# Performance work log

Measured on AMD Instinct MI355X. Metric: run time of the kernel, lower is better.

## Reference

```python
import jax, jax.numpy as jnp
import numpy as np

B, C, H, W = 2048, 256, 7, 7
EPS = 1e-6  # torch.nn.CosineSimilarity eps


def _masked_cos_loss(f1, f2, A):
    """Fused all-pairs masked cosine similarity.
    f1, f2: [B, C, H, W]; A: [H, W, H, W] binary mask.
    Replaces the original 7x7x7x7 Python loop of per-pixel CosineSimilarity calls.
    Returns per-batch loss [B]: sum_{ijkl: A==1} cos(f1[:,:,i,j], f2[:,:,k,l]) / (H*W*H*W).
    """
    n1 = jnp.linalg.norm(f1, axis=1)  # [B, H, W]
    n2 = jnp.linalg.norm(f2, axis=1)  # [B, H, W]
    dot = jnp.einsum('bcij,bckl->bijkl', f1, f2)  # [B, H, W, H, W]
    denom = jnp.maximum(n1[:, :, :, None, None] * n2[:, None, None, :, :], EPS)
    cos = dot / denom
    mask = (A == 1).astype(f1.dtype)
    return jnp.einsum('bijkl,ijkl->b', cos, mask) / (H * W * H * W)


def setup_inputs() -> dict:
    key = jax.random.key(0)
    k1, k2, k3, k4 = jax.random.split(key, 4)
    base_feature = jax.random.normal(k1, (B, C, H, W), dtype=jnp.float32)
    moment_feature = jax.random.normal(k2, (B, C, H, W), dtype=jnp.float32)
    base_A = jax.random.randint(k3, (H, W, H, W), 0, 2, dtype=jnp.int32)
    moment_A = jax.random.randint(k4, (H, W, H, W), 0, 2, dtype=jnp.int32)
    return {"base_feature": base_feature, "moment_feature": moment_feature,
            "base_A": base_A, "moment_A": moment_A}


def reference(base_feature, moment_feature, base_A, moment_A):
    # base_loss  = masked cos(base[i,j],   moment[k,l]) under base_A
    # moment_loss = masked cos(moment[i,j], base[k,l])  under moment_A
    base_loss = _masked_cos_loss(base_feature, moment_feature, base_A)
    moment_loss = _masked_cos_loss(moment_feature, base_feature, moment_A)
    return -base_loss - moment_loss  # [B]
```

## Files before the change

kernel.cpp:

```cpp
#include <hip/hip_runtime.h>
#include <math.h>


constexpr int NB     = 2048;
constexpr int NC     = 256;
constexpr int NP     = 49;
constexpr int SLAB_C = 8;
constexpr int PITCH  = 12;
constexpr int FWORDS = NP * PITCH;
constexpr int REGION = 1280;
constexpr int NSLABW = (NC / 2) / SLAB_C;
constexpr float EPS  = 1e-6f;

__global__ __launch_bounds__(256, 2)
void pixpro_kernel(const float* __restrict__ gbase,
                   const float* __restrict__ gmom,
                   const int*   __restrict__ A1,
                   const int*   __restrict__ A2,
                   float*       __restrict__ out)
{
    __shared__ unsigned char wtb[NP * NP];
    __shared__ __align__(16) float slab[4][REGION];

    const int tid  = threadIdx.x;
    const int wave = tid >> 6;
    const int lane = tid & 63;
    const int b    = blockIdx.x * 2 + (wave >> 1);
    const int half = wave & 1;

    for (int t = tid; t < NP * NP; t += 256) {
        int p = t / NP, q = t - p * NP;
        wtb[t] = (unsigned char)((A1[t] == 1 ? 1 : 0) + (A2[q * NP + p] == 1 ? 1 : 0));
    }
    __syncthreads();

    float* const sl  = slab[wave];
    float* const slb = sl;
    float* const slm = sl + FWORDS;

    const int lp = lane & 7, lq = lane >> 3;
    const int p0 = (lp < 7 ? lp : 6) * 7;
    const int q0 = (lq < 7 ? lq : 6) * 7;

    const float* gb = gbase + (size_t)b * (NC * NP) + (size_t)half * (128 * NP);
    const float* gm = gmom  + (size_t)b * (NC * NP) + (size_t)half * (128 * NP);

    const bool ld = (lane < NP);

    int wof[4];
    #pragma unroll
    for (int u = 0; u < 4; ++u) {
        int e  = 4 * lane + u;
        wof[u] = (e - 49 * (e / 49)) * PITCH + (e / 49);
    }

    const float* const vA = (lane < NP) ? (slb + lane * PITCH)
                                        : (slm + (lane - NP) * PITCH);
    const float* const vB = slm + ((lane < 34) ? (15 + lane) : 48) * PITCH;
    const float* const bp = slb + p0 * PITCH;
    const float* const mp = slm + q0 * PITCH;

    float acc[7][7];
    #pragma unroll
    for (int j = 0; j < 7; ++j)
        #pragma unroll
        for (int i = 0; i < 7; ++i) acc[j][i] = 0.0f;
    float nrm0 = 0.0f, nrm1 = 0.0f;

    float4 rb0 = {}, rb1 = {}, rm0 = {}, rm1 = {};
    if (ld) {
        const float4* pb = (const float4*)gb;
        const float4* pm = (const float4*)gm;
        rb0 = pb[lane]; rb1 = pb[lane + NP];
        rm0 = pm[lane]; rm1 = pm[lane + NP];
    }

    for (int s = 0; s < NSLABW; ++s) {
        if (ld) {
            slb[wof[0]]     = rb0.x; slb[wof[1]]     = rb0.y; slb[wof[2]]     = rb0.z; slb[wof[3]]     = rb0.w;
            slb[wof[0] + 4] = rb1.x; slb[wof[1] + 4] = rb1.y; slb[wof[2] + 4] = rb1.z; slb[wof[3] + 4] = rb1.w;
            slm[wof[0]]     = rm0.x; slm[wof[1]]     = rm0.y; slm[wof[2]]     = rm0.z; slm[wof[3]]     = rm0.w;
            slm[wof[0] + 4] = rm1.x; slm[wof[1] + 4] = rm1.y; slm[wof[2] + 4] = rm1.z; slm[wof[3] + 4] = rm1.w;
        }
        if (s + 1 < NSLABW && ld) {
            const float4* pb = (const float4*)(gb + (s + 1) * (SLAB_C * NP));
            const float4* pm = (const float4*)(gm + (s + 1) * (SLAB_C * NP));
            rb0 = pb[lane]; rb1 = pb[lane + NP];
            rm0 = pm[lane]; rm1 = pm[lane + NP];
        }
        asm volatile("s_waitcnt lgkmcnt(0)" ::: "memory");

        #pragma unroll
        for (int c0 = 0; c0 < SLAB_C; c0 += 4) {
            float4 mv[7];
            #pragma unroll
            for (int j = 0; j < 7; ++j)
                mv[j] = *(const float4*)(mp + j * PITCH + c0);
            float4 a4 = *(const float4*)(vA + c0);
            float4 b4 = *(const float4*)(vB + c0);
            nrm0 = fmaf(a4.x, a4.x, fmaf(a4.y, a4.y, fmaf(a4.z, a4.z, fmaf(a4.w, a4.w, nrm0))));
            nrm1 = fmaf(b4.x, b4.x, fmaf(b4.y, b4.y, fmaf(b4.z, b4.z, fmaf(b4.w, b4.w, nrm1))));
            #pragma unroll
            for (int i = 0; i < 7; ++i) {
                float4 bv = *(const float4*)(bp + i * PITCH + c0);
                #pragma unroll
                for (int j = 0; j < 7; ++j) {
                    float t0 = fmaf(bv.x, mv[j].x, acc[j][i]);
                    t0       = fmaf(bv.y, mv[j].y, t0);
                    t0       = fmaf(bv.z, mv[j].z, t0);
                    acc[j][i] = fmaf(bv.w, mv[j].w, t0);
                }
            }
        }
        asm volatile("s_waitcnt lgkmcnt(0)" ::: "memory");
    }

    __syncthreads();

    float* const ex   = slab[wave & ~1];
    const bool active = (lp < 7) && (lq < 7);
    const int  tix    = lq * 7 + lp;

    if (half) {
        ex[lane]      = nrm0;
        ex[64 + lane] = nrm1;
        if (active) {
            #pragma unroll
            for (int j = 0; j < 7; ++j)
                #pragma unroll
                for (int i = 0; i < 7; ++i)
                    ex[128 + tix * 49 + j * 7 + i] = acc[j][i];
        }
    }
    __syncthreads();

    if (!half) {
        nrm0 += ex[lane];
        nrm1 += ex[64 + lane];
        if (active) {
            #pragma unroll
            for (int j = 0; j < 7; ++j)
                #pragma unroll
                for (int i = 0; i < 7; ++i)
                    acc[j][i] += ex[128 + tix * 49 + j * 7 + i];
        }
        asm volatile("s_waitcnt lgkmcnt(0)" ::: "memory");

        ex[lane] = nrm0;
        if (lane < 34) ex[64 + lane] = nrm1;
        asm volatile("s_waitcnt lgkmcnt(0)" ::: "memory");

        float nbv[7], nmv[7];
        #pragma unroll
        for (int i = 0; i < 7; ++i) nbv[i] = sqrtf(ex[p0 + i]);
        #pragma unroll
        for (int j = 0; j < 7; ++j) nmv[j] = sqrtf(ex[NP + q0 + j]);

        float sum = 0.0f;
        if (active) {
            #pragma unroll
            for (int j = 0; j < 7; ++j)
                #pragma unroll
                for (int i = 0; i < 7; ++i) {
                    float w     = (float)wtb[(p0 + i) * NP + (q0 + j)];
                    float denom = fmaxf(nbv[i] * nmv[j], EPS);
                    sum += w * acc[j][i] / denom;
                }
        }
        #pragma unroll
        for (int m = 32; m; m >>= 1) sum += __shfl_xor(sum, m, 64);
        if (lane == 0) out[b] = sum * (-1.0f / 2401.0f);
    }
}

extern "C" void kernel_launch(void* const* d_in, const int* in_sizes, int n_in,
                              void* d_out, int out_size, void* d_ws, size_t ws_size,
                              hipStream_t stream)
{
    (void)in_sizes; (void)n_in; (void)d_ws; (void)ws_size; (void)out_size;
    const float* base = (const float*)d_in[0];
    const float* mom  = (const float*)d_in[1];
    const int*   A1   = (const int*)d_in[2];
    const int*   A2   = (const int*)d_in[3];
    float*       out  = (float*)d_out;

    pixpro_kernel<<<NB / 2, 256, 0, stream>>>(base, mom, A1, A2, out);
}
```

Measured before the change: 262.5 us.

## Double-buffer 4-channel LDS slabs with per-lane strided loads, dropping transpose scatter

Shrinks the per-wave LDS slab to 4 channels and keeps two LDS buffers (A and B) with their own register prefetches two slabs ahead. Each lane now loads one pixel's 4 channels with scalar strided global loads and stores them as one float4 into a pixel-major layout with pitch 4. This replaces the eight scattered scalar LDS writes of the old transpose. The goal is to cut LDS store instructions and bank conflicts and to overlap global loads with compute. In exchange, the global loads are no longer vectorised: each lane issues 4 separate dword loads per slab instead of 2 float4 loads.

```diff
diff --git a/kernel.cpp b/kernel.cpp
--- a/kernel.cpp
+++ b/kernel.cpp
@@ -5,9 +5,9 @@
 constexpr int NB     = 2048;
 constexpr int NC     = 256;
 constexpr int NP     = 49;
-constexpr int SLAB_C = 8;
-constexpr int PITCH  = 12;
-constexpr int FWORDS = NP * PITCH;
+constexpr int SLAB_C = 4;
+constexpr int FW     = NP * SLAB_C;
+constexpr int BUFW   = 2 * FW;
 constexpr int REGION = 1280;
 constexpr int NSLABW = (NC / 2) / SLAB_C;
 constexpr float EPS  = 1e-6f;
@@ -34,9 +34,7 @@
     }
     __syncthreads();
 
-    float* const sl  = slab[wave];
-    float* const slb = sl;
-    float* const slm = sl + FWORDS;
+    float* const sl = slab[wave];
 
     const int lp = lane & 7, lq = lane >> 3;
     const int p0 = (lp < 7 ? lp : 6) * 7;
@@ -44,21 +42,13 @@
 
     const float* gb = gbase + (size_t)b * (NC * NP) + (size_t)half * (128 * NP);
     const float* gm = gmom  + (size_t)b * (NC * NP) + (size_t)half * (128 * NP);
+    const float* gbl = gb + lane;
+    const float* gml = gm + lane;
 
     const bool ld = (lane < NP);
 
-    int wof[4];
-    #pragma unroll
-    for (int u = 0; u < 4; ++u) {
-        int e  = 4 * lane + u;
-        wof[u] = (e - 49 * (e / 49)) * PITCH + (e / 49);
-    }
-
-    const float* const vA = (lane < NP) ? (slb + lane * PITCH)
-                                        : (slm + (lane - NP) * PITCH);
-    const float* const vB = slm + ((lane < 34) ? (15 + lane) : 48) * PITCH;
-    const float* const bp = slb + p0 * PITCH;
-    const float* const mp = slm + q0 * PITCH;
+    const int vAw = (lane < NP) ? (4 * lane) : (FW + 4 * (lane - NP));
+    const int vBw = FW + 4 * ((lane < 34) ? (15 + lane) : 48);
 
     float acc[7][7];
     #pragma unroll
@@ -67,52 +57,63 @@
         for (int i = 0; i < 7; ++i) acc[j][i] = 0.0f;
     float nrm0 = 0.0f, nrm1 = 0.0f;
 
-    float4 rb0 = {}, rb1 = {}, rm0 = {}, rm1 = {};
+    float4 pbA = {}, pmA = {}, pbB = {}, pmB = {};
     if (ld) {
-        const float4* pb = (const float4*)gb;
-        const float4* pm = (const float4*)gm;
-        rb0 = pb[lane]; rb1 = pb[lane + NP];
-        rm0 = pm[lane]; rm1 = pm[lane + NP];
+        pbA.x = gbl[0];      pbA.y = gbl[NP];      pbA.z = gbl[2 * NP];      pbA.w = gbl[3 * NP];
+        pmA.x = gml[0];      pmA.y = gml[NP];      pmA.z = gml[2 * NP];      pmA.w = gml[3 * NP];
+        pbB.x = gbl[FW];     pbB.y = gbl[FW + NP]; pbB.z = gbl[FW + 2 * NP]; pbB.w = gbl[FW + 3 * NP];
+        pmB.x = gml[FW];     pmB.y = gml[FW + NP]; pmB.z = gml[FW + 2 * NP]; pmB.w = gml[FW + 3 * NP];
     }
 
-    for (int s = 0; s < NSLABW; ++s) {
+    auto compute = [&](int Boff) {
+        const float* base_ = sl + Boff;
+        float4 a4 = *(const float4*)(base_ + vAw);
+        float4 b4 = *(const float4*)(base_ + vBw);
+        nrm0 = fmaf(a4.x, a4.x, fmaf(a4.y, a4.y, fmaf(a4.z, a4.z, fmaf(a4.w, a4.w, nrm0))));
+        nrm1 = fmaf(b4.x, b4.x, fmaf(b4.y, b4.y, fmaf(b4.z, b4.z, fmaf(b4.w, b4.w, nrm1))));
+        float4 mv[7];
+        #pragma unroll
+        for (int j = 0; j < 7; ++j)
+            mv[j] = *(const float4*)(base_ + FW + q0 * 4 + 4 * j);
+        #pragma unroll
+        for (int i = 0; i < 7; ++i) {
+            float4 bv = *(const float4*)(base_ + p0 * 4 + 4 * i);
+            #pragma unroll
+            for (int j = 0; j < 7; ++j) {
+                float t0 = fmaf(bv.x, mv[j].x, acc[j][i]);
+                t0       = fmaf(bv.y, mv[j].y, t0);
+                t0       = fmaf(bv.z, mv[j].z, t0);
+                acc[j][i] = fmaf(bv.w, mv[j].w, t0);
+            }
+        }
+    };
+
+    for (int s = 0; s < NSLABW; s += 2) {
         if (ld) {
-            slb[wof[0]]     = rb0.x; slb[wof[1]]     = rb0.y; slb[wof[2]]     = rb0.z; slb[wof[3]]     = rb0.w;
-            slb[wof[0] + 4] = rb1.x; slb[wof[1] + 4] = rb1.y; slb[wof[2] + 4] = rb1.z; slb[wof[3] + 4] = rb1.w;
-            slm[wof[0]]     = rm0.x; slm[wof[1]]     = rm0.y; slm[wof[2]]     = rm0.z; slm[wof[3]]     = rm0.w;
-            slm[wof[0] + 4] = rm1.x; slm[wof[1] + 4] = rm1.y; slm[wof[2] + 4] = rm1.z; slm[wof[3] + 4] = rm1.w;
-        }
-        if (s + 1 < NSLABW && ld) {
-            const float4* pb = (const float4*)(gb + (s + 1) * (SLAB_C * NP));
-            const float4* pm = (const float4*)(gm + (s + 1) * (SLAB_C * NP));
-            rb0 = pb[lane]; rb1 = pb[lane + NP];
-            rm0 = pm[lane]; rm1 = pm[lane + NP];
-        }
-        asm volatile("s_waitcnt lgkmcnt(0)" ::: "memory");
-
-        #pragma unroll
-        for (int c0 = 0; c0 < SLAB_C; c0 += 4) {
-            float4 mv[7];
-            #pragma unroll
-            for (int j = 0; j < 7; ++j)
-                mv[j] = *(const float4*)(mp + j * PITCH + c0);
-            float4 a4 = *(const float4*)(vA + c0);
-            float4 b4 = *(const float4*)(vB + c0);
-            nrm0 = fmaf(a4.x, a4.x, fmaf(a4.y, a4.y, fmaf(a4.z, a4.z, fmaf(a4.w, a4.w, nrm0))));
-            nrm1 = fmaf(b4.x, b4.x, fmaf(b4.y, b4.y, fmaf(b4.z, b4.z, fmaf(b4.w, b4.w, nrm1))));
-            #pragma unroll
-            for (int i = 0; i < 7; ++i) {
-                float4 bv = *(const float4*)(bp + i * PITCH + c0);
-                #pragma unroll
-                for (int j = 0; j < 7; ++j) {
-                    float t0 = fmaf(bv.x, mv[j].x, acc[j][i]);
-                    t0       = fmaf(bv.y, mv[j].y, t0);
-                    t0       = fmaf(bv.z, mv[j].z, t0);
-                    acc[j][i] = fmaf(bv.w, mv[j].w, t0);
-                }
+            *(float4*)(sl + 4 * lane)      = pbA;
+            *(float4*)(sl + FW + 4 * lane) = pmA;
+            if (s + 2 < NSLABW) {
+                const float* pb_ = gbl + (s + 2) * FW;
+                const float* pm_ = gml + (s + 2) * FW;
+                pbA.x = pb_[0]; pbA.y = pb_[NP]; pbA.z = pb_[2 * NP]; pbA.w = pb_[3 * NP];
+                pmA.x = pm_[0]; pmA.y = pm_[NP]; pmA.z = pm_[2 * NP]; pmA.w = pm_[3 * NP];
             }
         }
         asm volatile("s_waitcnt lgkmcnt(0)" ::: "memory");
+        compute(0);
+
+        if (ld) {
+            *(float4*)(sl + BUFW + 4 * lane)      = pbB;
+            *(float4*)(sl + BUFW + FW + 4 * lane) = pmB;
+            if (s + 3 < NSLABW) {
+                const float* pb_ = gbl + (s + 3) * FW;
+                const float* pm_ = gml + (s + 3) * FW;
+                pbB.x = pb_[0]; pbB.y = pb_[NP]; pbB.z = pb_[2 * NP]; pbB.w = pb_[3 * NP];
+                pmB.x = pm_[0]; pmB.y = pm_[NP]; pmB.z = pm_[2 * NP]; pmB.w = pm_[3 * NP];
+            }
+        }
+        asm volatile("s_waitcnt lgkmcnt(0)" ::: "memory");
+        compute(BUFW);
     }
 
     __syncthreads();
```

Measured after the change: 248.4 us. -5.3%, faster.
